# Kernel optimization log

Measured on AMD Instinct MI355X. Metric: run time of the kernel, lower is better.

## Reference

```python
import jax, jax.numpy as jnp
import numpy as np

DIM = 768
HEADS = 12
HEAD_DIM = DIM // HEADS
SCALE = HEAD_DIM ** (-0.5)


def setup_inputs() -> dict:
    key = jax.random.key(0)
    k1, k2, k3, k4 = jax.random.split(key, 4)
    B, N = 2, 48 * 48
    x = jax.random.normal(k1, (B, N, DIM), dtype=jnp.float32)
    qkv_w = jax.random.normal(k2, (3 * DIM, DIM), dtype=jnp.float32) * (DIM ** -0.5)
    proj_w = jax.random.normal(k3, (DIM, DIM), dtype=jnp.float32) * (DIM ** -0.5)
    proj_b = jax.random.normal(k4, (DIM,), dtype=jnp.float32) * 0.02
    return {"x": x, "H": 48, "W": 48, "qkv_w": qkv_w, "proj_w": proj_w, "proj_b": proj_b}


def reference(x, H, W, qkv_w, proj_w, proj_b):
    B, N, C = x.shape
    h, d = HEADS, HEAD_DIM
    # qkv linear (no bias): [B,N,3C], then split into per-head q,k,v [B,h,N,d]
    qkv = jnp.einsum('bnc,fc->bnf', x, qkv_w)
    qkv = qkv.reshape(B, N, 3, h, d).transpose(2, 0, 3, 1, 4)
    q, k, v = qkv[0], qkv[1], qkv[2]
    attn = jnp.einsum('bhnd,bhmd->bhnm', q, k) * SCALE  # [B,h,N,N]
    attn = jax.nn.softmax(attn, axis=-1)
    out = jnp.einsum('bhnm,bhmd->bhnd', attn, v)  # [B,h,N,d]
    out = out.transpose(0, 2, 1, 3).reshape(B, N, C)
    out = jnp.einsum('bnc,fc->bnf', out, proj_w) + proj_b
    return out
```

## Files before the change

kernel.cpp:

```cpp
#include <hip/hip_runtime.h>

#define B_    2
#define N_    2304
#define C_    768
#define HEADS 12
#define D_    64
#define F3    2304
#define M_    (B_*N_)
#define SPLITS 2
#define KSPAN (N_/SPLITS)
#define QSCALE 0.18033688011112042f

typedef __attribute__((ext_vector_type(8)))  short bfrag;
typedef __attribute__((ext_vector_type(4)))  float ffrag;
typedef __attribute__((ext_vector_type(16))) float ffrag16;
typedef __attribute__((ext_vector_type(4)))  unsigned ufrag;
typedef __attribute__((ext_vector_type(2)))  unsigned uint2v;

__device__ __forceinline__ short f2bf(float f) {
    unsigned u = __float_as_uint(f);
    u += 0x7fff + ((u >> 16) & 1);
    return (short)(u >> 16);
}

__device__ __forceinline__ void gl2lds16(const void* g, void* l) {
    __builtin_amdgcn_global_load_lds(
        (const __attribute__((address_space(1))) void*)g,
        (__attribute__((address_space(3))) void*)l, 16, 0, 0);
}

__device__ __forceinline__ unsigned pktrunc(float a, float b) {
    return __builtin_amdgcn_perm(__float_as_uint(a), __float_as_uint(b),
                                 0x03020706u);
}

__global__ __launch_bounds__(256) void cast_all(const float* __restrict__ x,
                                                const float* __restrict__ qw,
                                                const float* __restrict__ pw,
                                                short* __restrict__ dst) {
    const int nx4 = (M_*C_)/4, nq4 = (F3*C_)/4, np4 = (C_*C_)/4;
    int i = blockIdx.x * 256 + threadIdx.x;
    if (i >= nx4 + nq4 + np4) return;
    const float* src; int off;
    if (i < nx4)            { src = x;  off = i; }
    else if (i < nx4 + nq4) { src = qw; off = i - nx4; }
    else                    { src = pw; off = i - nx4 - nq4; }
    float4 v = ((const float4*)src)[off];
    short4 o;
    o.x = f2bf(v.x); o.y = f2bf(v.y); o.z = f2bf(v.z); o.w = f2bf(v.w);
    ((short4*)dst)[i] = o;
}

__global__ __launch_bounds__(256) void qkv_gemm(const short* __restrict__ xb,
                                                const short* __restrict__ wb,
                                                short* __restrict__ Qb,
                                                short* __restrict__ Kb,
                                                short* __restrict__ Vtb) {
    __shared__ short As[2][128*32];
    __shared__ short Bs[2][128*32];
    const int t = threadIdx.x;
    const int w = t >> 6, lane = t & 63;
    const int quad = lane >> 4, l15 = lane & 15;
    const int wr = w >> 1, wc = w & 1;

    const int nwg = gridDim.x * gridDim.y;
    const int bid = blockIdx.y * gridDim.x + blockIdx.x;
    const int swz = (bid & 7) * (nwg >> 3) + (bid >> 3);
    const int m0 = (swz / gridDim.x) * 128, f0 = (swz % gridDim.x) * 128;

    const int srow = lane >> 2;
    const int skk  = (lane & 3) * 8;

    ffrag acc[4][4] = {};

    #pragma unroll
    for (int r = 0; r < 2; ++r) {
        int seg = r*4 + w;
        int row = seg*16 + srow;
        gl2lds16(xb + (size_t)(m0+row)*C_ + skk, As[0] + seg*512);
        gl2lds16(wb + (size_t)(f0+row)*C_ + skk, Bs[0] + seg*512);
    }
    __syncthreads();

    const int NKT = C_/32;
    for (int kt = 0; kt < NKT; ++kt) {
        const int cur = kt & 1;
        if (kt + 1 < NKT) {
            const int k0n = (kt+1)*32;
            #pragma unroll
            for (int r = 0; r < 2; ++r) {
                int seg = r*4 + w;
                int row = seg*16 + srow;
                gl2lds16(xb + (size_t)(m0+row)*C_ + k0n + skk, As[cur^1] + seg*512);
                gl2lds16(wb + (size_t)(f0+row)*C_ + k0n + skk, Bs[cur^1] + seg*512);
            }
        }
        bfrag af[4], bf[4];
        #pragma unroll
        for (int i = 0; i < 4; ++i)
            af[i] = *(const bfrag*)(As[cur] + (wr*64 + i*16 + l15)*32 + quad*8);
        #pragma unroll
        for (int j = 0; j < 4; ++j)
            bf[j] = *(const bfrag*)(Bs[cur] + (wc*64 + j*16 + l15)*32 + quad*8);
        #pragma unroll
        for (int i = 0; i < 4; ++i)
            #pragma unroll
            for (int j = 0; j < 4; ++j)
                acc[i][j] = __builtin_amdgcn_mfma_f32_16x16x32_bf16(af[i], bf[j], acc[i][j], 0, 0, 0);
        __syncthreads();
    }

    const int b   = m0 / N_;
    const int seg = f0 + wc*64;
    const int which = seg / C_;
    const int head  = (seg - which*C_) >> 6;
    const int bh    = b*HEADS + head;
    const int nbase = (m0 - b*N_) + wr*64 + quad*4;

    if (which == 0) {
        #pragma unroll
        for (int i = 0; i < 4; ++i) {
            int n0 = nbase + i*16;
            #pragma unroll
            for (int j = 0; j < 4; ++j) {
                int d = j*16 + l15;
                #pragma unroll
                for (int r = 0; r < 4; ++r)
                    Qb[((size_t)bh*N_ + n0 + r)*D_ + d] = f2bf(acc[i][j][r] * QSCALE);
            }
        }
    } else if (which == 1) {
        #pragma unroll
        for (int i = 0; i < 4; ++i) {
            int n0 = nbase + i*16;
            #pragma unroll
            for (int j = 0; j < 4; ++j) {
                int d = j*16 + l15;
                #pragma unroll
                for (int r = 0; r < 4; ++r)
                    Kb[((size_t)bh*N_ + n0 + r)*D_ + d] = f2bf(acc[i][j][r]);
            }
        }
    } else {
        #pragma unroll
        for (int i = 0; i < 4; ++i) {
            int n0 = nbase + i*16;
            #pragma unroll
            for (int j = 0; j < 4; ++j) {
                int d = j*16 + l15;
                short4 vv;
                vv.x = f2bf(acc[i][j][0]);
                vv.y = f2bf(acc[i][j][1]);
                vv.z = f2bf(acc[i][j][2]);
                vv.w = f2bf(acc[i][j][3]);
                *(short4*)(Vtb + ((size_t)bh*D_ + d)*N_ + n0) = vv;
            }
        }
    }
}

__global__ __launch_bounds__(256, 4) void attn_mfma(const short* __restrict__ Qb,
                                                    const short* __restrict__ Kb,
                                                    const short* __restrict__ Vtb,
                                                    float* __restrict__ Opart,
                                                    float* __restrict__ lpart) {
    __shared__ short lds[16384];
    const int t = threadIdx.x;
    const int w = t >> 6, lane = t & 63;
    const int l31 = lane & 31, hi = lane >> 5;
    const int bh = blockIdx.x, q0 = blockIdx.y * 128;
    const int split = blockIdx.z;
    const int kbase = split * KSPAN;
    const size_t base = (size_t)bh * N_ * D_;
    const int lrow = lane >> 3;
    const int lc   = (lane & 7) ^ lrow;

    short* Qs = lds + 8192;

    #pragma unroll
    for (int r = 0; r < 4; ++r) {
        int s = r*4 + w;
        gl2lds16(Qb + base + (size_t)(q0 + s*8 + lrow)*D_ + lc*8, Qs + s*512);
    }
    #pragma unroll
    for (int r = 0; r < 2; ++r) {
        int s = r*4 + w;
        int row = s*8 + lrow;
        gl2lds16(Kb  + base + (size_t)(kbase+row)*D_ + lc*8,    lds + s*512);
        gl2lds16(Vtb + (size_t)(bh*D_ + row)*N_ + kbase + lc*8, lds + 4096 + s*512);
    }
    __syncthreads();

    bfrag qf[4];
    {
        int row = w*32 + l31, r7 = row & 7;
        #pragma unroll
        for (int kc = 0; kc < 4; ++kc)
            qf[kc] = *(const bfrag*)(Qs + row*64 + ((kc*2 + hi) ^ r7)*8);
    }
    __syncthreads();

    bfrag vones;
    #pragma unroll
    for (int j = 0; j < 8; ++j) vones[j] = (short)0x3f80;

    ffrag16 oacc[2], lfr;
    #pragma unroll
    for (int r = 0; r < 16; ++r) { oacc[0][r] = 0.f; oacc[1][r] = 0.f; lfr[r] = 0.f; }

    const int NT = KSPAN / 64;
    for (int ti = 0; ti < NT; ++ti) {
        const int cur = ti & 1;
        const short* Kc = lds + cur*8192;
        const short* Vc = Kc + 4096;

        if (ti + 1 < NT) {
            short* Kn = lds + (cur^1)*8192;
            const int k0n = kbase + (ti+1)*64;
            #pragma unroll
            for (int r = 0; r < 2; ++r) {
                int s = r*4 + w;
                int row = s*8 + lrow;
                gl2lds16(Kb  + base + (size_t)(k0n+row)*D_ + lc*8,    Kn + s*512);
                gl2lds16(Vtb + (size_t)(bh*D_ + row)*N_ + k0n + lc*8, Kn + 4096 + s*512);
            }
        }

        ufrag pfr[4];
        #pragma unroll
        for (int kt = 0; kt < 2; ++kt) {
            ffrag16 s;
            #pragma unroll
            for (int r = 0; r < 16; ++r) s[r] = 0.f;
            int row = kt*32 + l31, r7 = row & 7;
            __builtin_amdgcn_s_setprio(1);
            #pragma unroll
            for (int kc = 0; kc < 4; ++kc) {
                bfrag kf = *(const bfrag*)(Kc + row*64 + ((kc*2 + hi) ^ r7)*8);
                s = __builtin_amdgcn_mfma_f32_32x32x16_bf16(kf, qf[kc], s, 0, 0, 0);
            }
            __builtin_amdgcn_s_setprio(0);
            #pragma unroll
            for (int r = 0; r < 16; ++r)
                s[r] = __builtin_amdgcn_exp2f(s[r]);
            unsigned q01_0 = pktrunc(s[0],  s[1]),  q23_0 = pktrunc(s[2],  s[3]);
            unsigned q01_1 = pktrunc(s[4],  s[5]),  q23_1 = pktrunc(s[6],  s[7]);
            unsigned q01_2 = pktrunc(s[8],  s[9]),  q23_2 = pktrunc(s[10], s[11]);
            unsigned q01_3 = pktrunc(s[12], s[13]), q23_3 = pktrunc(s[14], s[15]);
            uint2v e0 = __builtin_amdgcn_permlane32_swap(q01_0, q01_1, false, false);
            uint2v e1 = __builtin_amdgcn_permlane32_swap(q23_0, q23_1, false, false);
            uint2v e2 = __builtin_amdgcn_permlane32_swap(q01_2, q01_3, false, false);
            uint2v e3 = __builtin_amdgcn_permlane32_swap(q23_2, q23_3, false, false);
            ufrag lo, hif;
            lo[0]  = e0[0]; lo[1]  = e1[0]; lo[2]  = e0[1]; lo[3]  = e1[1];
            hif[0] = e2[0]; hif[1] = e3[0]; hif[2] = e2[1]; hif[3] = e3[1];
            pfr[kt*2]     = lo;
            pfr[kt*2 + 1] = hif;
        }

        __builtin_amdgcn_s_setprio(1);
        #pragma unroll
        for (int kc = 0; kc < 4; ++kc) {
            bfrag pf = __builtin_bit_cast(bfrag, pfr[kc]);
            #pragma unroll
            for (int dt = 0; dt < 2; ++dt) {
                int row = dt*32 + l31, r7 = row & 7;
                bfrag vf = *(const bfrag*)(Vc + row*64 + ((kc*2 + hi) ^ r7)*8);
                oacc[dt] = __builtin_amdgcn_mfma_f32_32x32x16_bf16(pf, vf, oacc[dt], 0, 0, 0);
            }
            lfr = __builtin_amdgcn_mfma_f32_32x32x16_bf16(pf, vones, lfr, 0, 0, 0);
        }
        __builtin_amdgcn_s_setprio(0);
        __syncthreads();
    }

    const int b = bh / HEADS, head = bh - b*HEADS;
    float* Op = Opart + (size_t)split * M_ * C_;
    float* lp = lpart + (size_t)split * (B_*HEADS) * N_;

    if (l31 == 0) {
        #pragma unroll
        for (int r = 0; r < 16; ++r) {
            int n = q0 + w*32 + (r & 3) + 8*(r >> 2) + 4*hi;
            lp[bh*N_ + n] = lfr[r];
        }
    }

    #pragma unroll
    for (int dt = 0; dt < 2; ++dt)
        #pragma unroll
        for (int r = 0; r < 16; ++r) {
            int n = q0 + w*32 + (r & 3) + 8*(r >> 2) + 4*hi;
            int c = head*D_ + dt*32 + l31;
            Op[((size_t)b*N_ + n)*C_ + c] = oacc[dt][r];
        }
}

__global__ __launch_bounds__(256) void attn_merge(const float* __restrict__ Opart,
                                                  const float* __restrict__ lpart,
                                                  short* __restrict__ Ob) {
    int i = blockIdx.x * 256 + threadIdx.x;
    int m = i / (C_/4);
    int c = (i - m*(C_/4)) * 4;
    int b = m / N_, n = m - b*N_;
    int bh = b*HEADS + (c >> 6);
    float4 o0 = ((const float4*)Opart)[i];
    float4 o1 = ((const float4*)(Opart + (size_t)M_*C_))[i];
    float l = lpart[bh*N_ + n] + lpart[(B_*HEADS)*N_ + bh*N_ + n];
    float inv = 1.f / l;
    short4 o;
    o.x = f2bf((o0.x + o1.x) * inv);
    o.y = f2bf((o0.y + o1.y) * inv);
    o.z = f2bf((o0.z + o1.z) * inv);
    o.w = f2bf((o0.w + o1.w) * inv);
    ((short4*)Ob)[i] = o;
}

__global__ __launch_bounds__(256) void proj_gemm(const short* __restrict__ Ab,
                                                 const short* __restrict__ wb,
                                                 const float* __restrict__ bias,
                                                 float* __restrict__ out) {
    __shared__ short As[2][128*32];
    __shared__ short Bs[2][128*32];
    const int t = threadIdx.x;
    const int w = t >> 6, lane = t & 63;
    const int quad = lane >> 4, l15 = lane & 15;
    const int wr = w >> 1, wc = w & 1;

    const int nwg = gridDim.x * gridDim.y;
    const int bid = blockIdx.y * gridDim.x + blockIdx.x;
    const int swz = (bid & 7) * (nwg >> 3) + (bid >> 3);
    const int m0 = (swz / gridDim.x) * 128, f0 = (swz % gridDim.x) * 128;

    const int srow = lane >> 2;
    const int skk  = (lane & 3) * 8;

    ffrag acc[4][4] = {};

    #pragma unroll
    for (int r = 0; r < 2; ++r) {
        int seg = r*4 + w;
        int row = seg*16 + srow;
        gl2lds16(Ab + (size_t)(m0+row)*C_ + skk, As[0] + seg*512);
        gl2lds16(wb + (size_t)(f0+row)*C_ + skk, Bs[0] + seg*512);
    }
    __syncthreads();

    const int NKT = C_/32;
    for (int kt = 0; kt < NKT; ++kt) {
        const int cur = kt & 1;
        if (kt + 1 < NKT) {
            const int k0n = (kt+1)*32;
            #pragma unroll
            for (int r = 0; r < 2; ++r) {
                int seg = r*4 + w;
                int row = seg*16 + srow;
                gl2lds16(Ab + (size_t)(m0+row)*C_ + k0n + skk, As[cur^1] + seg*512);
                gl2lds16(wb + (size_t)(f0+row)*C_ + k0n + skk, Bs[cur^1] + seg*512);
            }
        }
        bfrag af[4], bf[4];
        #pragma unroll
        for (int i = 0; i < 4; ++i)
            af[i] = *(const bfrag*)(As[cur] + (wr*64 + i*16 + l15)*32 + quad*8);
        #pragma unroll
        for (int j = 0; j < 4; ++j)
            bf[j] = *(const bfrag*)(Bs[cur] + (wc*64 + j*16 + l15)*32 + quad*8);
        #pragma unroll
        for (int i = 0; i < 4; ++i)
            #pragma unroll
            for (int j = 0; j < 4; ++j)
                acc[i][j] = __builtin_amdgcn_mfma_f32_16x16x32_bf16(af[i], bf[j], acc[i][j], 0, 0, 0);
        __syncthreads();
    }

    #pragma unroll
    for (int i = 0; i < 4; ++i) {
        int mbase = m0 + wr*64 + i*16 + quad*4;
        #pragma unroll
        for (int j = 0; j < 4; ++j) {
            int f = f0 + wc*64 + j*16 + l15;
            float bv = bias[f];
            #pragma unroll
            for (int r = 0; r < 4; ++r)
                out[(size_t)(mbase + r)*C_ + f] = acc[i][j][r] + bv;
        }
    }
}

extern "C" void kernel_launch(void* const* d_in, const int* in_sizes, int n_in,
                              void* d_out, int out_size, void* d_ws, size_t ws_size,
                              hipStream_t stream) {
    const float* x      = (const float*)d_in[0];
    const float* qkv_w  = (const float*)d_in[3];
    const float* proj_w = (const float*)d_in[4];
    const float* proj_b = (const float*)d_in[5];
    float* out = (float*)d_out;

    const size_t nx = (size_t)M_ * C_;
    const size_t nq = (size_t)F3 * C_;
    const size_t np = (size_t)C_ * C_;
    short* xb  = (short*)d_ws;
    short* qwb = xb  + nx;
    short* pwb = qwb + nq;
    short* Qb  = pwb + np;
    short* Kb  = Qb  + nx;
    short* Vtb = Kb  + nx;
    short* Ob  = Vtb + nx;
    float* Opart = (float*)(Ob + nx);
    float* lpart = Opart + (size_t)SPLITS * M_ * C_;

    const int ncast4 = (int)((nx + nq + np) / 4);
    cast_all<<<dim3((ncast4 + 255)/256), 256, 0, stream>>>(x, qkv_w, proj_w, xb);

    qkv_gemm<<<dim3(F3/128, M_/128), 256, 0, stream>>>(xb, qwb, Qb, Kb, Vtb);
    attn_mfma<<<dim3(B_*HEADS, N_/128, SPLITS), 256, 0, stream>>>(Qb, Kb, Vtb, Opart, lpart);
    attn_merge<<<dim3(((int)(nx/4) + 255)/256), 256, 0, stream>>>(Opart, lpart, Ob);
    proj_gemm<<<dim3(C_/128, M_/128), 256, 0, stream>>>(Ob, pwb, proj_b, out);
}
```

Measured before the change: 194.2 us.

## Split attention keys three ways and compute row sums with VALU instead of MFMA

Raises the key-dimension split of the attention kernel from two to three, giving more workgroups and a shorter per-block loop, and extends the merge kernel to sum three partial outputs and denominators. It also drops the extra MFMA against a ones vector that produced the softmax denominator, and instead accumulates bf16-truncated exponentials per lane, then combines the two half-waves with a shuffle. The trade-off is more partial-output memory traffic and merge work, plus extra VALU adds inside the inner loop. KSPAN is 768, which remains divisible by 64.

Measured after the change: 194.0 us. No clear change (-0.1%).

```diff
diff --git a/kernel.cpp b/kernel.cpp
--- a/kernel.cpp
+++ b/kernel.cpp
@@ -7,7 +7,7 @@
 #define D_    64
 #define F3    2304
 #define M_    (B_*N_)
-#define SPLITS 2
+#define SPLITS 3
 #define KSPAN (N_/SPLITS)
 #define QSCALE 0.18033688011112042f
 
@@ -32,6 +32,10 @@
 __device__ __forceinline__ unsigned pktrunc(float a, float b) {
     return __builtin_amdgcn_perm(__float_as_uint(a), __float_as_uint(b),
                                  0x03020706u);
+}
+
+__device__ __forceinline__ float btrunc(float a) {
+    return __uint_as_float(__float_as_uint(a) & 0xffff0000u);
 }
 
 __global__ __launch_bounds__(256) void cast_all(const float* __restrict__ x,
@@ -200,13 +204,10 @@
     }
     __syncthreads();
 
-    bfrag vones;
-    #pragma unroll
-    for (int j = 0; j < 8; ++j) vones[j] = (short)0x3f80;
-
-    ffrag16 oacc[2], lfr;
-    #pragma unroll
-    for (int r = 0; r < 16; ++r) { oacc[0][r] = 0.f; oacc[1][r] = 0.f; lfr[r] = 0.f; }
+    ffrag16 oacc[2];
+    #pragma unroll
+    for (int r = 0; r < 16; ++r) { oacc[0][r] = 0.f; oacc[1][r] = 0.f; }
+    float llane = 0.f;
 
     const int NT = KSPAN / 64;
     for (int ti = 0; ti < NT; ++ti) {
@@ -243,6 +244,15 @@
             #pragma unroll
             for (int r = 0; r < 16; ++r)
                 s[r] = __builtin_amdgcn_exp2f(s[r]);
+            {
+                float t0 = 0.f, t1 = 0.f;
+                #pragma unroll
+                for (int r = 0; r < 16; r += 2) {
+                    t0 += btrunc(s[r]);
+                    t1 += btrunc(s[r+1]);
+                }
+                llane += t0 + t1;
+            }
             unsigned q01_0 = pktrunc(s[0],  s[1]),  q23_0 = pktrunc(s[2],  s[3]);
             unsigned q01_1 = pktrunc(s[4],  s[5]),  q23_1 = pktrunc(s[6],  s[7]);
             unsigned q01_2 = pktrunc(s[8],  s[9]),  q23_2 = pktrunc(s[10], s[11]);
@@ -268,7 +278,6 @@
                 bfrag vf = *(const bfrag*)(Vc + row*64 + ((kc*2 + hi) ^ r7)*8);
                 oacc[dt] = __builtin_amdgcn_mfma_f32_32x32x16_bf16(pf, vf, oacc[dt], 0, 0, 0);
             }
-            lfr = __builtin_amdgcn_mfma_f32_32x32x16_bf16(pf, vones, lfr, 0, 0, 0);
         }
         __builtin_amdgcn_s_setprio(0);
         __syncthreads();
@@ -278,12 +287,11 @@
     float* Op = Opart + (size_t)split * M_ * C_;
     float* lp = lpart + (size_t)split * (B_*HEADS) * N_;
 
-    if (l31 == 0) {
-        #pragma unroll
-        for (int r = 0; r < 16; ++r) {
-            int n = q0 + w*32 + (r & 3) + 8*(r >> 2) + 4*hi;
-            lp[bh*N_ + n] = lfr[r];
-        }
+    {
+        float lpart_other = __shfl_xor(llane, 32, 64);
+        float ltot = llane + lpart_other;
+        if (hi == 0)
+            lp[bh*N_ + q0 + w*32 + l31] = ltot;
     }
 
     #pragma unroll
@@ -304,15 +312,17 @@
     int c = (i - m*(C_/4)) * 4;
     int b = m / N_, n = m - b*N_;
     int bh = b*HEADS + (c >> 6);
+    const int LP = (B_*HEADS)*N_;
     float4 o0 = ((const float4*)Opart)[i];
     float4 o1 = ((const float4*)(Opart + (size_t)M_*C_))[i];
-    float l = lpart[bh*N_ + n] + lpart[(B_*HEADS)*N_ + bh*N_ + n];
+    float4 o2 = ((const float4*)(Opart + 2*(size_t)M_*C_))[i];
+    float l = lpart[bh*N_ + n] + lpart[LP + bh*N_ + n] + lpart[2*LP + bh*N_ + n];
     float inv = 1.f / l;
     short4 o;
-    o.x = f2bf((o0.x + o1.x) * inv);
-    o.y = f2bf((o0.y + o1.y) * inv);
-    o.z = f2bf((o0.z + o1.z) * inv);
-    o.w = f2bf((o0.w + o1.w) * inv);
+    o.x = f2bf((o0.x + o1.x + o2.x) * inv);
+    o.y = f2bf((o0.y + o1.y + o2.y) * inv);
+    o.z = f2bf((o0.z + o1.z + o2.z) * inv);
+    o.w = f2bf((o0.w + o1.w + o2.w) * inv);
     ((short4*)Ob)[i] = o;
 }
 
```

## Use partial vmcnt waits with raw barriers and swizzle attention block order

Applied to the files above, without the earlier changes.

All three MFMA kernels drop __syncthreads, which waits for all outstanding loads, and instead issue s_waitcnt vmcnt(4) so only the current tile's global-to-LDS loads must finish while the next tile's prefetch stays in flight, followed by a raw s_barrier. The attention grid is also transposed and workgroup IDs are swizzled in groups of 8 so blocks sharing a head's K/V run close together for cache reuse. The hand-written waitcnt relies on the exact count of outstanding loads per thread and may race if the compiler reorders memory ops or LDS reads are not fenced.

Measured after the change: 194.4 us. Within noise of the previous version (+0.1%).

```diff
diff --git a/kernel.cpp b/kernel.cpp
--- a/kernel.cpp
+++ b/kernel.cpp
@@ -28,6 +28,9 @@
         (const __attribute__((address_space(1))) void*)g,
         (__attribute__((address_space(3))) void*)l, 16, 0, 0);
 }
+
+__device__ __forceinline__ void wait_vm4() { asm volatile("s_waitcnt vmcnt(4)" ::: "memory"); }
+__device__ __forceinline__ void wait_vm0() { asm volatile("s_waitcnt vmcnt(0)" ::: "memory"); }
 
 __device__ __forceinline__ unsigned pktrunc(float a, float b) {
     return __builtin_amdgcn_perm(__float_as_uint(a), __float_as_uint(b),
@@ -80,7 +83,6 @@
         gl2lds16(xb + (size_t)(m0+row)*C_ + skk, As[0] + seg*512);
         gl2lds16(wb + (size_t)(f0+row)*C_ + skk, Bs[0] + seg*512);
     }
-    __syncthreads();
 
     const int NKT = C_/32;
     for (int kt = 0; kt < NKT; ++kt) {
@@ -94,7 +96,12 @@
                 gl2lds16(xb + (size_t)(m0+row)*C_ + k0n + skk, As[cur^1] + seg*512);
                 gl2lds16(wb + (size_t)(f0+row)*C_ + k0n + skk, Bs[cur^1] + seg*512);
             }
-        }
+            wait_vm4();
+        } else {
+            wait_vm0();
+        }
+        __builtin_amdgcn_s_barrier();
+
         bfrag af[4], bf[4];
         #pragma unroll
         for (int i = 0; i < 4; ++i)
@@ -107,7 +114,7 @@
             #pragma unroll
             for (int j = 0; j < 4; ++j)
                 acc[i][j] = __builtin_amdgcn_mfma_f32_16x16x32_bf16(af[i], bf[j], acc[i][j], 0, 0, 0);
-        __syncthreads();
+        __builtin_amdgcn_s_barrier();
     }
 
     const int b   = m0 / N_;
@@ -168,7 +175,13 @@
     const int t = threadIdx.x;
     const int w = t >> 6, lane = t & 63;
     const int l31 = lane & 31, hi = lane >> 5;
-    const int bh = blockIdx.x, q0 = blockIdx.y * 128;
+
+    const int nwg = gridDim.x * gridDim.y;
+    const int fid = blockIdx.y * gridDim.x + blockIdx.x;
+    const int swz = (fid & 7) * (nwg >> 3) + (fid >> 3);
+    const int bh  = swz / gridDim.x;
+    const int q0  = (swz - bh * gridDim.x) * 128;
+
     const int split = blockIdx.z;
     const int kbase = split * KSPAN;
     const size_t base = (size_t)bh * N_ * D_;
@@ -224,7 +237,11 @@
                 gl2lds16(Kb  + base + (size_t)(k0n+row)*D_ + lc*8,    Kn + s*512);
                 gl2lds16(Vtb + (size_t)(bh*D_ + row)*N_ + k0n + lc*8, Kn + 4096 + s*512);
             }
-        }
+            wait_vm4();
+        } else {
+            wait_vm0();
+        }
+        __builtin_amdgcn_s_barrier();
 
         ufrag pfr[4];
         #pragma unroll
@@ -271,7 +288,7 @@
             lfr = __builtin_amdgcn_mfma_f32_32x32x16_bf16(pf, vones, lfr, 0, 0, 0);
         }
         __builtin_amdgcn_s_setprio(0);
-        __syncthreads();
+        __builtin_amdgcn_s_barrier();
     }
 
     const int b = bh / HEADS, head = bh - b*HEADS;
@@ -344,7 +361,6 @@
         gl2lds16(Ab + (size_t)(m0+row)*C_ + skk, As[0] + seg*512);
         gl2lds16(wb + (size_t)(f0+row)*C_ + skk, Bs[0] + seg*512);
     }
-    __syncthreads();
 
     const int NKT = C_/32;
     for (int kt = 0; kt < NKT; ++kt) {
@@ -358,7 +374,12 @@
                 gl2lds16(Ab + (size_t)(m0+row)*C_ + k0n + skk, As[cur^1] + seg*512);
                 gl2lds16(wb + (size_t)(f0+row)*C_ + k0n + skk, Bs[cur^1] + seg*512);
             }
-        }
+            wait_vm4();
+        } else {
+            wait_vm0();
+        }
+        __builtin_amdgcn_s_barrier();
+
         bfrag af[4], bf[4];
         #pragma unroll
         for (int i = 0; i < 4; ++i)
@@ -371,7 +392,7 @@
             #pragma unroll
             for (int j = 0; j < 4; ++j)
                 acc[i][j] = __builtin_amdgcn_mfma_f32_16x16x32_bf16(af[i], bf[j], acc[i][j], 0, 0, 0);
-        __syncthreads();
+        __builtin_amdgcn_s_barrier();
     }
 
     #pragma unroll
@@ -414,7 +435,7 @@
     cast_all<<<dim3((ncast4 + 255)/256), 256, 0, stream>>>(x, qkv_w, proj_w, xb);
 
     qkv_gemm<<<dim3(F3/128, M_/128), 256, 0, stream>>>(xb, qwb, Qb, Kb, Vtb);
-    attn_mfma<<<dim3(B_*HEADS, N_/128, SPLITS), 256, 0, stream>>>(Qb, Kb, Vtb, Opart, lpart);
+    attn_mfma<<<dim3(N_/128, B_*HEADS, SPLITS), 256, 0, stream>>>(Qb, Kb, Vtb, Opart, lpart);
     attn_merge<<<dim3(((int)(nx/4) + 255)/256), 256, 0, stream>>>(Opart, lpart, Ob);
     proj_gemm<<<dim3(C_/128, M_/128), 256, 0, stream>>>(Ob, pwb, proj_b, out);
 }
```
